# Kernel optimization log

Measured on AMD Instinct MI355X. Metric: run time of the kernel, lower is better.

## Reference

```python
import jax, jax.numpy as jnp
import numpy as np

ALPHA = 0.2  # LeakyReLU negative slope

B, K, F = 64, 100, 128   # batch, window_size (=num_nodes), n_features
E = 2 * K                 # embed_dim*2 = 200 (embed_dim defaults to window_size)


def setup_inputs() -> dict:
    key = jax.random.key(0)
    k1, k2, k3, k4, k5 = jax.random.split(key, 5)
    x = jax.random.normal(k1, (B, K, F), dtype=jnp.float32)
    # lin: Linear(2F -> E); store weight as (2F, E) so projection is x @ W
    W = jax.random.normal(k2, (2 * F, E), dtype=jnp.float32) * (1.0 / np.sqrt(2 * F))
    b = jax.random.normal(k3, (E,), dtype=jnp.float32) * 0.01
    # attention vector a: (E, 1) in torch; use (E,)
    a = jax.random.normal(k4, (E,), dtype=jnp.float32) * (1.414 / np.sqrt(E))
    bias = jax.random.normal(k5, (K, K), dtype=jnp.float32) * 0.01
    return {"x": x, "W": W, "b": b, "a": a, "bias": bias}


def reference(x, W, b, a, bias):
    F_ = x.shape[-1]
    # lin(concat(left, right)) == left @ W[:F] + right @ W[F:] + b;
    # compute the two projections once each instead of materializing the
    # (B, K, K, 2F) pairwise concat tensor.
    left_p = jnp.einsum('bkf,fe->bke', x, W[:F_])    # (B, K, E)
    right_p = jnp.einsum('bkf,fe->bke', x, W[F_:])   # (B, K, E)
    pre = left_p[:, :, None, :] + right_p[:, None, :, :] + b  # (B, K, K, E)
    act = jnp.where(pre > 0, pre, ALPHA * pre)                # LeakyReLU
    e = jnp.einsum('bije,e->bij', act, a) + bias              # (B, K, K)
    attention = jax.nn.softmax(e, axis=2)
    h = jax.nn.sigmoid(jnp.einsum('bij,bjf->bif', attention, x))  # (B, K, F)
    return h
```

## Files before the change

### kernel.cpp

```cpp
#include <hip/hip_runtime.h>

typedef _Float16 half_t;
typedef _Float16 h2 __attribute__((ext_vector_type(2)));
typedef unsigned int uint32;

#define K_ 100
#define F_ 128
#define E_ 200

#if defined(__has_builtin)
#if __has_builtin(__builtin_amdgcn_fdot2)
#define FDOT2(a,b,c) __builtin_amdgcn_fdot2((a),(b),(c),false)
#endif
#endif
#ifndef FDOT2
#define FDOT2(a,b,c) fmaf((float)(a).y,(float)(b).y, fmaf((float)(a).x,(float)(b).x,(c)))
#endif

__device__ __forceinline__ h2 bch2(uint32 u){ return __builtin_bit_cast(h2,u); }
__device__ __forceinline__ uint32 pkh2(float a, float b){
  h2 p; p.x=(half_t)a; p.y=(half_t)b; return __builtin_bit_cast(uint32,p);
}

#define LH_OFF 0
#define RH_OFF 640000
#define AH_OFF 1280000
#define AL_OFF 1280128
#define AR_OFF 1286528
#define XJ_OFF 1292928

__global__ __launch_bounds__(256) void k_proj(
    const float* __restrict__ x, const float* __restrict__ W,
    const float* __restrict__ bvec, const float* __restrict__ avec,
    uint32* __restrict__ ws)
{
  const int t  = threadIdx.x;
  const int r0 = (int)blockIdx.x * 10;

  __shared__ __align__(16) uint32 xsh[10 * 64];
  __shared__ float red[20][100];
  __shared__ float red2[20 * 10];

  for (int u = t; u < 640; u += 256) {
    int row = u >> 6, f2 = u & 63;
    const float* xp = x + (size_t)(r0 + row) * F_ + 2 * f2;
    xsh[row * 64 + f2] = pkh2(xp[0], xp[1]);
  }
  if (blockIdx.x == 0 && t < 100)
    ws[AH_OFF + t] = pkh2(avec[2*t], avec[2*t+1]);
  __syncthreads();

  for (int u = t; u < 640; u += 256) {
    int f = u & 127, lp = u >> 7;
    uint32 u0 = xsh[(2*lp)     * 64 + (f >> 1)];
    uint32 u1 = xsh[(2*lp + 1) * 64 + (f >> 1)];
    int sh = (f & 1) * 16;
    ws[XJ_OFF + (size_t)(r0/2 + lp) * 128 + f] =
        ((u0 >> sh) & 0xffffu) | (((u1 >> sh) & 0xffffu) << 16);
  }

  if (t < 200) {
    const bool isR = (t >= 100);
    const int e2 = isR ? (t - 100) : t;
    const float* Wp = W + (size_t)(isR ? 128 : 0) * E_ + 2 * e2;

    float acc0[10], acc1[10];
    #pragma unroll
    for (int r = 0; r < 10; ++r) { acc0[r] = 0.f; acc1[r] = 0.f; }

    #pragma unroll
    for (int q = 0; q < 16; ++q) {
      uint32 w0u[4], w1u[4];
      #pragma unroll
      for (int fp = 0; fp < 4; ++fp) {
        const float* p0 = Wp + (size_t)(8*q + 2*fp) * E_;
        float2 Av = *(const float2*)p0;
        float2 Bv = *(const float2*)(p0 + E_);
        w0u[fp] = pkh2(Av.x, Bv.x);
        w1u[fp] = pkh2(Av.y, Bv.y);
      }
      #pragma unroll
      for (int r = 0; r < 10; ++r) {
        uint4 xq = *(const uint4*)(xsh + r * 64 + 4 * q);
        acc0[r] = FDOT2(bch2(xq.x), bch2(w0u[0]), acc0[r]);
        acc0[r] = FDOT2(bch2(xq.y), bch2(w0u[1]), acc0[r]);
        acc0[r] = FDOT2(bch2(xq.z), bch2(w0u[2]), acc0[r]);
        acc0[r] = FDOT2(bch2(xq.w), bch2(w0u[3]), acc0[r]);
        acc1[r] = FDOT2(bch2(xq.x), bch2(w1u[0]), acc1[r]);
        acc1[r] = FDOT2(bch2(xq.y), bch2(w1u[1]), acc1[r]);
        acc1[r] = FDOT2(bch2(xq.z), bch2(w1u[2]), acc1[r]);
        acc1[r] = FDOT2(bch2(xq.w), bch2(w1u[3]), acc1[r]);
      }
    }
    if (isR) {
      float b0 = bvec[2 * e2], b1 = bvec[2 * e2 + 1];
      #pragma unroll
      for (int r = 0; r < 10; ++r) { acc0[r] += b0; acc1[r] += b1; }
    }
    h2 a2 = bch2(pkh2(avec[2*e2], avec[2*e2+1]));
    uint32* dst = ws + (isR ? RH_OFF : LH_OFF);
    #pragma unroll
    for (int r = 0; r < 10; ++r) {
      uint32 pr = pkh2(acc0[r], acc1[r]);
      dst[(size_t)(r0 + r) * 100 + e2] = pr;
      red[(isR ? 10 : 0) + r][e2] = FDOT2(a2, bch2(pr), 0.f);
    }
  }
  __syncthreads();

  if (t < 200) {
    int rr = t / 10, seg = t % 10;
    const float* rp = red[rr] + seg * 10;
    float s = 0.f;
    #pragma unroll
    for (int k = 0; k < 10; ++k) s += rp[k];
    red2[rr * 10 + seg] = s;
  }
  __syncthreads();
  if (t < 20) {
    float s = 0.f;
    #pragma unroll
    for (int k = 0; k < 10; ++k) s += red2[t * 10 + k];
    float* dstf = (float*)(ws + (t >= 10 ? AR_OFF : AL_OFF));
    dstf[r0 + (t % 10)] = s;
  }
}

#define STEPA(A_, lu, au, ru)                                              \
  do {                                                                     \
    h2 mm = __builtin_elementwise_min(bch2(lu) + bch2(ru), z2);            \
    A_ = FDOT2(bch2(au), mm, A_);                                          \
  } while (0)

#define RPAD 104
#define LPAD 108

__global__ __launch_bounds__(256) void k_main(
    const float* __restrict__ x, const float* __restrict__ bias,
    const uint32* __restrict__ ws, float* __restrict__ out)
{
  const int t  = threadIdx.x;
  const int i0 = (int)blockIdx.x * 20;
  const int b  = (int)blockIdx.y;

  __shared__ __align__(16) uint32 Rsh[100 * RPAD];
  __shared__ __align__(16) uint32 Lsh[20 * LPAD];
  __shared__ uint32 Ash[100];
  __shared__ float  att[20 * 100];
  __shared__ uint32 att2[20 * 50];
  __shared__ float  scratch[512];
  __shared__ float  rowmax[20], rowinv[20];

  const bool act = (t < 250);
  const int iq = act ? (t % 10) : 0;
  const int tj = act ? (t / 10) : 0;

  {
    const uint32* Rb = ws + RH_OFF + (size_t)b * K_ * 100;
    for (int u = t; u < 2500; u += 256) {
      int row = u / 25, c4 = (u % 25) * 4;
      *(uint4*)(&Rsh[row * RPAD + c4]) = *(const uint4*)(Rb + (size_t)row * 100 + c4);
    }
    const uint32* Lb = ws + LH_OFF + (size_t)(b * K_ + i0) * 100;
    for (int u = t; u < 500; u += 256) {
      int row = u / 25, c4 = (u % 25) * 4;
      *(uint4*)(&Lsh[row * LPAD + c4]) = *(const uint4*)(Lb + (size_t)row * 100 + c4);
    }
    if (t < 100) Ash[t] = ws[AH_OFF + t];
  }
  __syncthreads();

  float acc[2][4];
  #pragma unroll
  for (int p = 0; p < 2; ++p)
    #pragma unroll
    for (int s = 0; s < 4; ++s) acc[p][s] = 0.f;
  h2 z2; z2.x = (half_t)0; z2.y = (half_t)0;

  if (act) {
    const uint32* Lp0 = Lsh + (2*iq)     * LPAD;
    const uint32* Lp1 = Lsh + (2*iq + 1) * LPAD;
    const uint32* Rp0 = Rsh + tj * RPAD;
    const uint32* Rp1 = Rsh + (tj + 25) * RPAD;
    const uint32* Rp2 = Rsh + (tj + 50) * RPAD;
    const uint32* Rp3 = Rsh + (tj + 75) * RPAD;
    #pragma unroll 5
    for (int q = 0; q < 25; ++q) {
      uint4 L0q = *(const uint4*)(Lp0 + 4*q);
      uint4 L1q = *(const uint4*)(Lp1 + 4*q);
      uint4 Aq  = *(const uint4*)(Ash + 4*q);
      uint4 R0q = *(const uint4*)(Rp0 + 4*q);
      uint4 R1q = *(const uint4*)(Rp1 + 4*q);
      uint4 R2q = *(const uint4*)(Rp2 + 4*q);
      uint4 R3q = *(const uint4*)(Rp3 + 4*q);
      STEPA(acc[0][0], L0q.x, Aq.x, R0q.x); STEPA(acc[0][1], L0q.x, Aq.x, R1q.x);
      STEPA(acc[0][2], L0q.x, Aq.x, R2q.x); STEPA(acc[0][3], L0q.x, Aq.x, R3q.x);
      STEPA(acc[1][0], L1q.x, Aq.x, R0q.x); STEPA(acc[1][1], L1q.x, Aq.x, R1q.x);
      STEPA(acc[1][2], L1q.x, Aq.x, R2q.x); STEPA(acc[1][3], L1q.x, Aq.x, R3q.x);
      STEPA(acc[0][0], L0q.y, Aq.y, R0q.y); STEPA(acc[0][1], L0q.y, Aq.y, R1q.y);
      STEPA(acc[0][2], L0q.y, Aq.y, R2q.y); STEPA(acc[0][3], L0q.y, Aq.y, R3q.y);
      STEPA(acc[1][0], L1q.y, Aq.y, R0q.y); STEPA(acc[1][1], L1q.y, Aq.y, R1q.y);
      STEPA(acc[1][2], L1q.y, Aq.y, R2q.y); STEPA(acc[1][3], L1q.y, Aq.y, R3q.y);
      STEPA(acc[0][0], L0q.z, Aq.z, R0q.z); STEPA(acc[0][1], L0q.z, Aq.z, R1q.z);
      STEPA(acc[0][2], L0q.z, Aq.z, R2q.z); STEPA(acc[0][3], L0q.z, Aq.z, R3q.z);
      STEPA(acc[1][0], L1q.z, Aq.z, R0q.z); STEPA(acc[1][1], L1q.z, Aq.z, R1q.z);
      STEPA(acc[1][2], L1q.z, Aq.z, R2q.z); STEPA(acc[1][3], L1q.z, Aq.z, R3q.z);
      STEPA(acc[0][0], L0q.w, Aq.w, R0q.w); STEPA(acc[0][1], L0q.w, Aq.w, R1q.w);
      STEPA(acc[0][2], L0q.w, Aq.w, R2q.w); STEPA(acc[0][3], L0q.w, Aq.w, R3q.w);
      STEPA(acc[1][0], L1q.w, Aq.w, R0q.w); STEPA(acc[1][1], L1q.w, Aq.w, R1q.w);
      STEPA(acc[1][2], L1q.w, Aq.w, R2q.w); STEPA(acc[1][3], L1q.w, Aq.w, R3q.w);
    }
  }

  float v[2][4];
  if (act) {
    const float* ALf = (const float*)(ws + AL_OFF);
    const float* ARf = (const float*)(ws + AR_OFF);
    float al0 = ALf[b*K_ + i0 + 2*iq];
    float al1 = ALf[b*K_ + i0 + 2*iq + 1];
    #pragma unroll
    for (int s = 0; s < 4; ++s) {
      int j = tj + 25*s;
      float arj = ARf[b*K_ + j];
      float lv0 = al0 + arj + bias[(i0 + 2*iq)*K_ + j]     - 0.8f*acc[0][s];
      float lv1 = al1 + arj + bias[(i0 + 2*iq + 1)*K_ + j] - 0.8f*acc[1][s];
      v[0][s] = fminf(fmaxf(lv0, -30000.f), 30000.f);
      v[1][s] = fminf(fmaxf(lv1, -30000.f), 30000.f);
    }
  }

  {
    float m0 = -3.0e38f, m1 = -3.0e38f;
    if (act) {
      #pragma unroll
      for (int s = 0; s < 4; ++s) { m0 = fmaxf(m0, v[0][s]); m1 = fmaxf(m1, v[1][s]); }
    }
    scratch[t] = m0; scratch[256 + t] = m1;
    __syncthreads();
    if (t < 20) {
      int p = t & 1, iqr = t >> 1;
      const float* sp = scratch + p*256 + iqr;
      float mm = sp[0];
      for (int k = 1; k < 25; ++k) mm = fmaxf(mm, sp[10*k]);
      rowmax[t] = mm;
    }
    __syncthreads();
    float e0 = 0.f, e1 = 0.f;
    if (act) {
      float ma = rowmax[2*iq], mb = rowmax[2*iq + 1];
      #pragma unroll
      for (int s = 0; s < 4; ++s) { e0 += __expf(v[0][s] - ma); e1 += __expf(v[1][s] - mb); }
    }
    scratch[t] = e0; scratch[256 + t] = e1;
    __syncthreads();
    if (t < 20) {
      int p = t & 1, iqr = t >> 1;
      const float* sp = scratch + p*256 + iqr;
      float s2 = 0.f;
      for (int k = 0; k < 25; ++k) s2 += sp[10*k];
      rowinv[t] = 1.f / s2;
    }
    __syncthreads();
  }
  if (act) {
    #pragma unroll
    for (int p = 0; p < 2; ++p) {
      int row = 2*iq + p;
      float m = rowmax[row], inv = rowinv[row];
      #pragma unroll
      for (int s = 0; s < 4; ++s)
        att[row*K_ + tj + 25*s] = __expf(v[p][s] - m) * inv;
    }
  }
  __syncthreads();
  for (int u = t; u < 1000; u += 256) {
    int i = u / 50, jp = u - i*50;
    att2[i*50 + jp] = pkh2(att[i*K_ + 2*jp], att[i*K_ + 2*jp + 1]);
  }
  __syncthreads();

  {
    const int f = t & 127, ig = t >> 7;
    const uint32* XJ = ws + XJ_OFF + (size_t)(b*50) * 128;
    float z[10];
    #pragma unroll
    for (int m = 0; m < 10; ++m) z[m] = 0.f;
    for (int jp = 0; jp < 50; ++jp) {
      h2 xv = bch2(XJ[jp*128 + f]);
      #pragma unroll
      for (int m = 0; m < 10; ++m) {
        h2 av = bch2(att2[(ig*10 + m)*50 + jp]);
        z[m] = FDOT2(av, xv, z[m]);
      }
    }
    #pragma unroll
    for (int m = 0; m < 10; ++m) {
      int i = ig*10 + m;
      out[(size_t)(b*K_ + i0 + i)*F_ + f] = 1.f / (1.f + __expf(-z[m]));
    }
  }
}

extern "C" void kernel_launch(void* const* d_in, const int* in_sizes, int n_in,
                              void* d_out, int out_size, void* d_ws, size_t ws_size,
                              hipStream_t stream)
{
  const float* x    = (const float*)d_in[0];
  const float* W    = (const float*)d_in[1];
  const float* bvec = (const float*)d_in[2];
  const float* avec = (const float*)d_in[3];
  const float* bias = (const float*)d_in[4];
  float* out  = (float*)d_out;
  uint32* ws  = (uint32*)d_ws;

  k_proj<<<dim3(640),   dim3(256), 0, stream>>>(x, W, bvec, avec, ws);
  k_main<<<dim3(5, 64), dim3(256), 0, stream>>>(x, bias, ws, out);
}
```

Measured before the change: 103.8 us.

## Halve rows per block to double grid size, drop LDS padding and A staging

Each k_main block now handles 10 query rows instead of 20, which doubles the grid to 640 blocks and halves per-thread accumulators (2x2 instead of 2x4). The padded LDS rows for R/L are removed in favour of a flat contiguous uint4 copy, and the attention vector is read directly from global memory instead of staged in LDS. This aims for better CU occupancy and less register pressure. In exchange, every block reloads the full 100x100 R tile, so R loading per row doubles, and dropping the padding may introduce LDS bank conflicts.

```diff
diff --git a/kernel.cpp b/kernel.cpp
--- a/kernel.cpp
+++ b/kernel.cpp
@@ -132,95 +132,71 @@
     A_ = FDOT2(bch2(au), mm, A_);                                          \
   } while (0)
 
-#define RPAD 104
-#define LPAD 108
-
 __global__ __launch_bounds__(256) void k_main(
     const float* __restrict__ x, const float* __restrict__ bias,
     const uint32* __restrict__ ws, float* __restrict__ out)
 {
   const int t  = threadIdx.x;
-  const int i0 = (int)blockIdx.x * 20;
+  const int i0 = (int)blockIdx.x * 10;
   const int b  = (int)blockIdx.y;
 
-  __shared__ __align__(16) uint32 Rsh[100 * RPAD];
-  __shared__ __align__(16) uint32 Lsh[20 * LPAD];
-  __shared__ uint32 Ash[100];
-  __shared__ float  att[20 * 100];
-  __shared__ uint32 att2[20 * 50];
+  __shared__ __align__(16) uint32 Rsh[100 * 100];
+  __shared__ __align__(16) uint32 Lsh[10 * 100];
+  __shared__ float  att[10 * 100];
+  __shared__ uint32 att2[10 * 50];
   __shared__ float  scratch[512];
-  __shared__ float  rowmax[20], rowinv[20];
+  __shared__ float  rowmax[10], rowinv[10];
 
   const bool act = (t < 250);
-  const int iq = act ? (t % 10) : 0;
-  const int tj = act ? (t / 10) : 0;
+  const int iq = act ? (t % 5) : 0;
+  const int tj = act ? (t / 5) : 0;
 
   {
-    const uint32* Rb = ws + RH_OFF + (size_t)b * K_ * 100;
-    for (int u = t; u < 2500; u += 256) {
-      int row = u / 25, c4 = (u % 25) * 4;
-      *(uint4*)(&Rsh[row * RPAD + c4]) = *(const uint4*)(Rb + (size_t)row * 100 + c4);
-    }
-    const uint32* Lb = ws + LH_OFF + (size_t)(b * K_ + i0) * 100;
-    for (int u = t; u < 500; u += 256) {
-      int row = u / 25, c4 = (u % 25) * 4;
-      *(uint4*)(&Lsh[row * LPAD + c4]) = *(const uint4*)(Lb + (size_t)row * 100 + c4);
-    }
-    if (t < 100) Ash[t] = ws[AH_OFF + t];
-  }
-  __syncthreads();
-
-  float acc[2][4];
-  #pragma unroll
-  for (int p = 0; p < 2; ++p)
-    #pragma unroll
-    for (int s = 0; s < 4; ++s) acc[p][s] = 0.f;
+    const uint4* Rb4 = (const uint4*)(ws + RH_OFF + (size_t)b * K_ * 100);
+    for (int u = t; u < 2500; u += 256)
+      *(uint4*)(&Rsh[u * 4]) = Rb4[u];
+    const uint4* Lb4 = (const uint4*)(ws + LH_OFF + (size_t)(b * K_ + i0) * 100);
+    if (t < 250)
+      *(uint4*)(&Lsh[t * 4]) = Lb4[t];
+  }
+  __syncthreads();
+
+  float acc[2][2] = {{0.f,0.f},{0.f,0.f}};
   h2 z2; z2.x = (half_t)0; z2.y = (half_t)0;
 
   if (act) {
-    const uint32* Lp0 = Lsh + (2*iq)     * LPAD;
-    const uint32* Lp1 = Lsh + (2*iq + 1) * LPAD;
-    const uint32* Rp0 = Rsh + tj * RPAD;
-    const uint32* Rp1 = Rsh + (tj + 25) * RPAD;
-    const uint32* Rp2 = Rsh + (tj + 50) * RPAD;
-    const uint32* Rp3 = Rsh + (tj + 75) * RPAD;
+    const uint4* Ag  = (const uint4*)(ws + AH_OFF);
+    const uint32* Lp0 = Lsh + (2*iq)     * 100;
+    const uint32* Lp1 = Lsh + (2*iq + 1) * 100;
+    const uint32* Rp0 = Rsh + tj * 100;
+    const uint32* Rp1 = Rsh + (tj + 50) * 100;
     #pragma unroll 5
     for (int q = 0; q < 25; ++q) {
+      uint4 Aq  = Ag[q];
       uint4 L0q = *(const uint4*)(Lp0 + 4*q);
       uint4 L1q = *(const uint4*)(Lp1 + 4*q);
-      uint4 Aq  = *(const uint4*)(Ash + 4*q);
       uint4 R0q = *(const uint4*)(Rp0 + 4*q);
       uint4 R1q = *(const uint4*)(Rp1 + 4*q);
-      uint4 R2q = *(const uint4*)(Rp2 + 4*q);
-      uint4 R3q = *(const uint4*)(Rp3 + 4*q);
       STEPA(acc[0][0], L0q.x, Aq.x, R0q.x); STEPA(acc[0][1], L0q.x, Aq.x, R1q.x);
-      STEPA(acc[0][2], L0q.x, Aq.x, R2q.x); STEPA(acc[0][3], L0q.x, Aq.x, R3q.x);
       STEPA(acc[1][0], L1q.x, Aq.x, R0q.x); STEPA(acc[1][1], L1q.x, Aq.x, R1q.x);
-      STEPA(acc[1][2], L1q.x, Aq.x, R2q.x); STEPA(acc[1][3], L1q.x, Aq.x, R3q.x);
       STEPA(acc[0][0], L0q.y, Aq.y, R0q.y); STEPA(acc[0][1], L0q.y, Aq.y, R1q.y);
-      STEPA(acc[0][2], L0q.y, Aq.y, R2q.y); STEPA(acc[0][3], L0q.y, Aq.y, R3q.y);
       STEPA(acc[1][0], L1q.y, Aq.y, R0q.y); STEPA(acc[1][1], L1q.y, Aq.y, R1q.y);
-      STEPA(acc[1][2], L1q.y, Aq.y, R2q.y); STEPA(acc[1][3], L1q.y, Aq.y, R3q.y);
       STEPA(acc[0][0], L0q.z, Aq.z, R0q.z); STEPA(acc[0][1], L0q.z, Aq.z, R1q.z);
-      STEPA(acc[0][2], L0q.z, Aq.z, R2q.z); STEPA(acc[0][3], L0q.z, Aq.z, R3q.z);
       STEPA(acc[1][0], L1q.z, Aq.z, R0q.z); STEPA(acc[1][1], L1q.z, Aq.z, R1q.z);
-      STEPA(acc[1][2], L1q.z, Aq.z, R2q.z); STEPA(acc[1][3], L1q.z, Aq.z, R3q.z);
       STEPA(acc[0][0], L0q.w, Aq.w, R0q.w); STEPA(acc[0][1], L0q.w, Aq.w, R1q.w);
-      STEPA(acc[0][2], L0q.w, Aq.w, R2q.w); STEPA(acc[0][3], L0q.w, Aq.w, R3q.w);
       STEPA(acc[1][0], L1q.w, Aq.w, R0q.w); STEPA(acc[1][1], L1q.w, Aq.w, R1q.w);
-      STEPA(acc[1][2], L1q.w, Aq.w, R2q.w); STEPA(acc[1][3], L1q.w, Aq.w, R3q.w);
-    }
-  }
-
-  float v[2][4];
+    }
+  }
+
+  float v[2][2];
   if (act) {
     const float* ALf = (const float*)(ws + AL_OFF);
     const float* ARf = (const float*)(ws + AR_OFF);
     float al0 = ALf[b*K_ + i0 + 2*iq];
     float al1 = ALf[b*K_ + i0 + 2*iq + 1];
     #pragma unroll
-    for (int s = 0; s < 4; ++s) {
-      int j = tj + 25*s;
+    for (int s = 0; s < 2; ++s) {
+      int j = tj + 50*s;
       float arj = ARf[b*K_ + j];
       float lv0 = al0 + arj + bias[(i0 + 2*iq)*K_ + j]     - 0.8f*acc[0][s];
       float lv1 = al1 + arj + bias[(i0 + 2*iq + 1)*K_ + j] - 0.8f*acc[1][s];
@@ -232,32 +208,32 @@
   {
     float m0 = -3.0e38f, m1 = -3.0e38f;
     if (act) {
-      #pragma unroll
-      for (int s = 0; s < 4; ++s) { m0 = fmaxf(m0, v[0][s]); m1 = fmaxf(m1, v[1][s]); }
+      m0 = fmaxf(v[0][0], v[0][1]);
+      m1 = fmaxf(v[1][0], v[1][1]);
     }
     scratch[t] = m0; scratch[256 + t] = m1;
     __syncthreads();
-    if (t < 20) {
+    if (t < 10) {
       int p = t & 1, iqr = t >> 1;
       const float* sp = scratch + p*256 + iqr;
       float mm = sp[0];
-      for (int k = 1; k < 25; ++k) mm = fmaxf(mm, sp[10*k]);
+      for (int k = 1; k < 50; ++k) mm = fmaxf(mm, sp[5*k]);
       rowmax[t] = mm;
     }
     __syncthreads();
     float e0 = 0.f, e1 = 0.f;
     if (act) {
       float ma = rowmax[2*iq], mb = rowmax[2*iq + 1];
-      #pragma unroll
-      for (int s = 0; s < 4; ++s) { e0 += __expf(v[0][s] - ma); e1 += __expf(v[1][s] - mb); }
+      e0 = __expf(v[0][0] - ma) + __expf(v[0][1] - ma);
+      e1 = __expf(v[1][0] - mb) + __expf(v[1][1] - mb);
     }
     scratch[t] = e0; scratch[256 + t] = e1;
     __syncthreads();
-    if (t < 20) {
+    if (t < 10) {
       int p = t & 1, iqr = t >> 1;
       const float* sp = scratch + p*256 + iqr;
       float s2 = 0.f;
-      for (int k = 0; k < 25; ++k) s2 += sp[10*k];
+      for (int k = 0; k < 50; ++k) s2 += sp[5*k];
       rowinv[t] = 1.f / s2;
     }
     __syncthreads();
@@ -267,13 +243,12 @@
     for (int p = 0; p < 2; ++p) {
       int row = 2*iq + p;
       float m = rowmax[row], inv = rowinv[row];
-      #pragma unroll
-      for (int s = 0; s < 4; ++s)
-        att[row*K_ + tj + 25*s] = __expf(v[p][s] - m) * inv;
-    }
-  }
-  __syncthreads();
-  for (int u = t; u < 1000; u += 256) {
+      att[row*K_ + tj]      = __expf(v[p][0] - m) * inv;
+      att[row*K_ + tj + 50] = __expf(v[p][1] - m) * inv;
+    }
+  }
+  __syncthreads();
+  for (int u = t; u < 500; u += 256) {
     int i = u / 50, jp = u - i*50;
     att2[i*50 + jp] = pkh2(att[i*K_ + 2*jp], att[i*K_ + 2*jp + 1]);
   }
@@ -282,20 +257,20 @@
   {
     const int f = t & 127, ig = t >> 7;
     const uint32* XJ = ws + XJ_OFF + (size_t)(b*50) * 128;
-    float z[10];
-    #pragma unroll
-    for (int m = 0; m < 10; ++m) z[m] = 0.f;
+    float z[5];
+    #pragma unroll
+    for (int m = 0; m < 5; ++m) z[m] = 0.f;
     for (int jp = 0; jp < 50; ++jp) {
       h2 xv = bch2(XJ[jp*128 + f]);
       #pragma unroll
-      for (int m = 0; m < 10; ++m) {
-        h2 av = bch2(att2[(ig*10 + m)*50 + jp]);
+      for (int m = 0; m < 5; ++m) {
+        h2 av = bch2(att2[(ig*5 + m)*50 + jp]);
         z[m] = FDOT2(av, xv, z[m]);
       }
     }
     #pragma unroll
-    for (int m = 0; m < 10; ++m) {
-      int i = ig*10 + m;
+    for (int m = 0; m < 5; ++m) {
+      int i = ig*5 + m;
       out[(size_t)(b*K_ + i0 + i)*F_ + f] = 1.f / (1.f + __expf(-z[m]));
     }
   }
@@ -313,6 +288,6 @@
   float* out  = (float*)d_out;
   uint32* ws  = (uint32*)d_ws;
 
-  k_proj<<<dim3(640),   dim3(256), 0, stream>>>(x, W, bvec, avec, ws);
-  k_main<<<dim3(5, 64), dim3(256), 0, stream>>>(x, bias, ws, out);
-}
+  k_proj<<<dim3(640),    dim3(256), 0, stream>>>(x, W, bvec, avec, ws);
+  k_main<<<dim3(10, 64), dim3(256), 0, stream>>>(x, bias, ws, out);
+}
```

Result: faster. 98.38 us (-5.2%).
